# Performance work log

Measured on AMD Instinct MI355X. Metric: run time of the kernel, lower is better.

The kernel has to match this reference:

```python
import jax, jax.numpy as jnp
import numpy as np

N = 100000      # nodes
E = 1600000     # edges (avg degree 16)
D_IN = 128
CONV_SIZES = [64, 64]
FC_SIZES = [64, 32, 1]


def _glorot(key, shape):
    lim = np.sqrt(6.0 / (shape[0] + shape[1]))
    return jax.random.uniform(key, shape, jnp.float32, -lim, lim)


def setup_inputs() -> dict:
    key = jax.random.key(0)
    ks = jax.random.split(key, 2 + len(CONV_SIZES) + len(FC_SIZES))
    inp = {
        "x": jax.random.normal(ks[0], (N, D_IN), jnp.float32),
        "edge_index": jax.random.randint(ks[1], (2, E), 0, N, dtype=jnp.int64),
    }
    size = D_IN
    ki = 2
    for li, s in enumerate(CONV_SIZES):
        inp[f"cW{li}"] = _glorot(ks[ki], (size, s)); ki += 1
        inp[f"cb{li}"] = jnp.zeros((s,), jnp.float32)
        size = s
    for li, s in enumerate(FC_SIZES):
        inp[f"fW{li}"] = _glorot(ks[ki], (size, s)); ki += 1
        inp[f"fb{li}"] = jnp.zeros((s,), jnp.float32)
        size = s
    return inp


def gcn_conv(x, src, dst, W, b, n_nodes):
    """PyG GCNConv: symmetric normalization with added self-loops."""
    xl = x @ W  # [N, out]
    # degree including self-loop
    deg = jnp.zeros((n_nodes,), xl.dtype).at[dst].add(1.0) + 1.0
    dinv = jax.lax.rsqrt(deg)
    norm = dinv[src] * dinv[dst]                 # [E]
    msg = xl[src] * norm[:, None]                # gather + scale, [E, out]
    agg = jax.ops.segment_sum(msg, dst, num_segments=n_nodes)
    # self-loop contribution: norm = 1/deg
    return agg + xl * (1.0 / deg)[:, None] + b


def reference(x, edge_index, cW0, cb0, cW1, cb1, fW0, fb0, fW1, fb1, fW2, fb2):
    src, dst = edge_index[0], edge_index[1]
    h = jnp.tanh(gcn_conv(x, src, dst, cW0, cb0, N))
    h = jnp.tanh(gcn_conv(h, src, dst, cW1, cb1, N))
    h = jnp.tanh(h @ fW0 + fb0)
    h = jnp.tanh(h @ fW1 + fb1)
    return h @ fW2 + fb2  # [N, 1]
```

## Files before the change

kernel.cpp:

```cpp
#include <hip/hip_runtime.h>
#include <math.h>

#define N_NODES 100000
#define N_EDGES 1600000
#define NB     391
#define CHUNK  4096
#define NBLK_A 391

typedef unsigned short ushort_t;
typedef __attribute__((ext_vector_type(2))) float f2v;

__device__ inline unsigned short f2bf(float f) {
    unsigned u = __float_as_uint(f);
    unsigned r = (u + 0x7FFFu + ((u >> 16) & 1u)) >> 16;
    return (unsigned short)r;
}
__device__ inline void accp(f2v& a, unsigned u) {
    f2v t;
    t.x = __uint_as_float(u << 16);
    t.y = __uint_as_float(u & 0xFFFF0000u);
    a += t;
}
__device__ inline float fast_tanh(float x) {
    float e = __expf(2.0f * x);
    return fmaf(-2.0f, __builtin_amdgcn_rcpf(e + 1.0f), 1.0f);
}
__device__ inline void fma4(float4& acc, const float4 a,
                            const float4 w0, const float4 w1,
                            const float4 w2, const float4 w3) {
    acc.x = fmaf(a.x, w0.x, fmaf(a.y, w1.x, fmaf(a.z, w2.x, fmaf(a.w, w3.x, acc.x))));
    acc.y = fmaf(a.x, w0.y, fmaf(a.y, w1.y, fmaf(a.z, w2.y, fmaf(a.w, w3.y, acc.y))));
    acc.z = fmaf(a.x, w0.z, fmaf(a.y, w1.z, fmaf(a.z, w2.z, fmaf(a.w, w3.z, acc.z))));
    acc.w = fmaf(a.x, w0.w, fmaf(a.y, w1.w, fmaf(a.z, w2.w, fmaf(a.w, w3.w, acc.w))));
}


__global__ __launch_bounds__(256) void k_count(const int* __restrict__ dst,
                                               unsigned* __restrict__ cnt) {
    __shared__ unsigned h[NB];
    const int tid = threadIdx.x;
    const long e0 = (long)blockIdx.x * CHUNK;
    for (int i = tid; i < NB; i += 256) h[i] = 0u;
    __syncthreads();
    for (int i = tid; i < CHUNK; i += 256) {
        long e = e0 + i;
        if (e < N_EDGES) atomicAdd(&h[((unsigned)dst[e]) >> 8], 1u);
    }
    __syncthreads();
    for (int b = tid; b < NB; b += 256) cnt[b * NBLK_A + blockIdx.x] = h[b];
}

__global__ __launch_bounds__(512) void k_bucket_scan(unsigned* __restrict__ cnt,
                                                     unsigned* __restrict__ btot) {
    __shared__ unsigned s[512];
    const int tid = threadIdx.x;
    const int b = blockIdx.x;
    unsigned v = (tid < NBLK_A) ? cnt[b * NBLK_A + tid] : 0u;
    s[tid] = v;
    __syncthreads();
    for (int o = 1; o < 512; o <<= 1) {
        unsigned t = (tid >= o) ? s[tid - o] : 0u;
        __syncthreads();
        s[tid] += t;
        __syncthreads();
    }
    if (tid < NBLK_A) cnt[b * NBLK_A + tid] = s[tid] - v;
    if (tid == NBLK_A - 1) btot[b] = s[tid];
}

__global__ __launch_bounds__(512) void k_scan_bkt(const unsigned* __restrict__ btot,
                                                  unsigned* __restrict__ bktbase) {
    __shared__ unsigned s[512];
    const int tid = threadIdx.x;
    unsigned v = (tid < NB) ? btot[tid] : 0u;
    s[tid] = v;
    __syncthreads();
    for (int o = 1; o < 512; o <<= 1) {
        unsigned t = (tid >= o) ? s[tid - o] : 0u;
        __syncthreads();
        s[tid] += t;
        __syncthreads();
    }
    if (tid < NB) bktbase[tid] = s[tid] - v;
    if (tid == NB - 1) bktbase[NB] = s[tid];
}

__global__ __launch_bounds__(256) void k_bin(const int* __restrict__ src,
                                             const int* __restrict__ dst,
                                             const unsigned* __restrict__ cnt,
                                             const unsigned* __restrict__ bktbase,
                                             unsigned* __restrict__ binned) {
    __shared__ unsigned cntA[NB];
    __shared__ unsigned excl[NB];
    __shared__ unsigned gbase[NB];
    __shared__ unsigned scanbuf[512];
    __shared__ unsigned data[CHUNK];
    const int tid = threadIdx.x;
    const long e0 = (long)blockIdx.x * CHUNK;

    for (int i = tid; i < NB; i += 256) cntA[i] = 0u;
    __syncthreads();
    for (int i = tid; i < CHUNK; i += 256) {
        long e = e0 + i;
        if (e < N_EDGES) atomicAdd(&cntA[((unsigned)dst[e]) >> 8], 1u);
    }
    __syncthreads();
    scanbuf[tid] = (tid < NB) ? cntA[tid] : 0u;
    scanbuf[tid + 256] = (tid + 256 < NB) ? cntA[tid + 256] : 0u;
    __syncthreads();
    for (int o = 1; o < 512; o <<= 1) {
        unsigned v0 = (tid >= o) ? scanbuf[tid - o] : 0u;
        unsigned v1 = (tid + 256 >= o) ? scanbuf[tid + 256 - o] : 0u;
        __syncthreads();
        scanbuf[tid] += v0;
        scanbuf[tid + 256] += v1;
        __syncthreads();
    }
    for (int b = tid; b < NB; b += 256) {
        excl[b] = scanbuf[b] - cntA[b];
        gbase[b] = bktbase[b] + cnt[b * NBLK_A + blockIdx.x];
    }
    __syncthreads();
    for (int i = tid; i < NB; i += 256) cntA[i] = 0u;
    __syncthreads();
    for (int i = tid; i < CHUNK; i += 256) {
        long e = e0 + i;
        if (e < N_EDGES) {
            unsigned d = (unsigned)dst[e];
            unsigned b = d >> 8;
            unsigned slot = excl[b] + atomicAdd(&cntA[b], 1u);
            data[slot] = (((unsigned)src[e]) << 8) | (d & 255u);
        }
    }
    __syncthreads();
    const int w = tid >> 6, lane = tid & 63;
    for (int b = w; b < NB; b += 4) {
        unsigned c = cntA[b];
        unsigned sb = excl[b], gb = gbase[b];
        for (unsigned k = lane; k < c; k += 64)
            binned[gb + k] = data[sb + k];
    }
}

__global__ __launch_bounds__(256) void k_csr_fill2(const unsigned* __restrict__ binned,
                                                   const unsigned* __restrict__ bktbase,
                                                   unsigned* __restrict__ rowptr,
                                                   float* __restrict__ dinv,
                                                   int* __restrict__ ssrc) {
    __shared__ unsigned cnt[256];
    __shared__ unsigned s[256];
    __shared__ unsigned cur[256];
    const int b = blockIdx.x;
    const int tid = threadIdx.x;
    const int n0 = b * 256;
    const unsigned beg = bktbase[b], end = bktbase[b + 1];
    cnt[tid] = 0u;
    __syncthreads();
    for (unsigned i = beg + tid; i < end; i += 256)
        atomicAdd(&cnt[binned[i] & 255u], 1u);
    __syncthreads();
    const unsigned v = cnt[tid];
    s[tid] = v;
    __syncthreads();
    for (int o = 1; o < 256; o <<= 1) {
        unsigned t = (tid >= o) ? s[tid - o] : 0u;
        __syncthreads();
        s[tid] += t;
        __syncthreads();
    }
    const unsigned excl = s[tid] - v;
    const int node = n0 + tid;
    if (node < N_NODES) {
        rowptr[node] = beg + excl;
        dinv[node] = rsqrtf((float)(v + 1u));
        if (node == N_NODES - 1) rowptr[N_NODES] = end;
    }
    cur[tid] = beg + excl;
    __syncthreads();
    for (unsigned i = beg + tid; i < end; i += 256) {
        unsigned p = binned[i];
        unsigned pos = atomicAdd(&cur[p & 255u], 1u);
        ssrc[pos] = (int)(p >> 8);
    }
}


template<int K>
__global__ __launch_bounds__(256) void k_gemm_bf(const float* __restrict__ A,
                                                 const float* __restrict__ W,
                                                 const float* __restrict__ dinv,
                                                 ushort_t* __restrict__ C) {
    constexpr int OUT = 64;
    constexpr int BR = 64;
    constexpr int LDA = K + 4;
    __shared__ float Wld[K * OUT];
    __shared__ float Ald[BR * LDA];
    const int tid = threadIdx.x;
    const int row0 = blockIdx.x * BR;
    const int nrows = (N_NODES - row0 < BR) ? (N_NODES - row0) : BR;

    {
        const float4* W4 = reinterpret_cast<const float4*>(W);
        float4* Wl4 = reinterpret_cast<float4*>(Wld);
        for (int i = tid; i < K * OUT / 4; i += 256) Wl4[i] = W4[i];
        const float4* A4 = reinterpret_cast<const float4*>(A + (size_t)row0 * K);
        const int nv = nrows * (K / 4);
        for (int i = tid; i < nv; i += 256) {
            int r = i / (K / 4), q = i % (K / 4);
            *reinterpret_cast<float4*>(&Ald[r * LDA + q * 4]) = A4[i];
        }
    }
    __syncthreads();

    const int tr = tid >> 4;
    const int tc = tid & 15;
    const int r0 = tr * 4;
    float4 acc0 = {0,0,0,0}, acc1 = {0,0,0,0}, acc2 = {0,0,0,0}, acc3 = {0,0,0,0};
#pragma unroll 2
    for (int k4 = 0; k4 < K; k4 += 4) {
        const float4 a0 = *reinterpret_cast<const float4*>(&Ald[(r0 + 0) * LDA + k4]);
        const float4 a1 = *reinterpret_cast<const float4*>(&Ald[(r0 + 1) * LDA + k4]);
        const float4 a2 = *reinterpret_cast<const float4*>(&Ald[(r0 + 2) * LDA + k4]);
        const float4 a3 = *reinterpret_cast<const float4*>(&Ald[(r0 + 3) * LDA + k4]);
        const float4 w0 = *reinterpret_cast<const float4*>(&Wld[(k4 + 0) * OUT + tc * 4]);
        const float4 w1 = *reinterpret_cast<const float4*>(&Wld[(k4 + 1) * OUT + tc * 4]);
        const float4 w2 = *reinterpret_cast<const float4*>(&Wld[(k4 + 2) * OUT + tc * 4]);
        const float4 w3 = *reinterpret_cast<const float4*>(&Wld[(k4 + 3) * OUT + tc * 4]);
        fma4(acc0, a0, w0, w1, w2, w3);
        fma4(acc1, a1, w0, w1, w2, w3);
        fma4(acc2, a2, w0, w1, w2, w3);
        fma4(acc3, a3, w0, w1, w2, w3);
    }
    float4 accs[4] = {acc0, acc1, acc2, acc3};
#pragma unroll
    for (int i = 0; i < 4; ++i) {
        const int r = r0 + i;
        if (r < nrows) {
            const float di = dinv[row0 + r];
            ushort4 o;
            o.x = f2bf(accs[i].x * di);
            o.y = f2bf(accs[i].y * di);
            o.z = f2bf(accs[i].z * di);
            o.w = f2bf(accs[i].w * di);
            *reinterpret_cast<ushort4*>(&C[(size_t)(row0 + r) * OUT + tc * 4]) = o;
        }
    }
}

__global__ __launch_bounds__(256) void k_agg(const ushort_t* __restrict__ xlb,
                                             const float* __restrict__ dinv,
                                             const unsigned* __restrict__ rowptr,
                                             const int* __restrict__ ssrc,
                                             const float* __restrict__ bias,
                                             float* __restrict__ h) {
    const int node = blockIdx.x * 4 + (threadIdx.x >> 6);
    const int lane = threadIdx.x & 63;
    const int g = lane >> 4;
    const int l = lane & 15;
    const uint2* xb2 = reinterpret_cast<const uint2*>(xlb);

    const unsigned beg = rowptr[node], end = rowptr[node + 1];
    f2v a0 = {0.f, 0.f}, a1 = {0.f, 0.f};
    f2v b0 = {0.f, 0.f}, b1 = {0.f, 0.f};
    if (g == 0) {
        const uint2 v = xb2[(size_t)node * 16 + l];
        accp(a0, v.x); accp(a1, v.y);
    }
    unsigned j = beg + g;
    for (; j + 12 < end; j += 16) {
        const int s0i = ssrc[j];
        const int s1i = ssrc[j + 4];
        const int s2i = ssrc[j + 8];
        const int s3i = ssrc[j + 12];
        const uint2 v0 = xb2[(size_t)s0i * 16 + l];
        const uint2 v1 = xb2[(size_t)s1i * 16 + l];
        const uint2 v2 = xb2[(size_t)s2i * 16 + l];
        const uint2 v3 = xb2[(size_t)s3i * 16 + l];
        accp(a0, v0.x); accp(a1, v0.y);
        accp(b0, v1.x); accp(b1, v1.y);
        accp(a0, v2.x); accp(a1, v2.y);
        accp(b0, v3.x); accp(b1, v3.y);
    }
    for (; j < end; j += 4) {
        const uint2 v = xb2[(size_t)ssrc[j] * 16 + l];
        accp(a0, v.x); accp(a1, v.y);
    }
    a0 += b0; a1 += b1;
    float s0 = a0.x, s1 = a0.y, s2 = a1.x, s3 = a1.y;
    s0 += __shfl_xor(s0, 16); s1 += __shfl_xor(s1, 16);
    s2 += __shfl_xor(s2, 16); s3 += __shfl_xor(s3, 16);
    s0 += __shfl_xor(s0, 32); s1 += __shfl_xor(s1, 32);
    s2 += __shfl_xor(s2, 32); s3 += __shfl_xor(s3, 32);
    const float t01 = (g & 1) ? s1 : s0;
    const float t23 = (g & 1) ? s3 : s2;
    const float v = (g & 2) ? t23 : t01;
    const int f = l * 4 + g;
    const float r = fast_tanh(fmaf(v, dinv[node], bias[f]));
    h[(size_t)node * 64 + f] = r;
}

__global__ __launch_bounds__(256, 4) void k_fc(const float* __restrict__ h2,
                                               const float* __restrict__ fW0, const float* __restrict__ fb0,
                                               const float* __restrict__ fW1, const float* __restrict__ fb1,
                                               const float* __restrict__ fW2, const float* __restrict__ fb2,
                                               float* __restrict__ out) {
    constexpr int BR = 32;
    constexpr int LDH = 68;
    __shared__ float W0[64 * 64];
    __shared__ float W1[64 * 32];
    __shared__ float Hin[BR * LDH];
    __shared__ float Ht[BR * LDH];
    __shared__ float Hs[BR * 33];
    __shared__ float W2s[33];
    const int tid = threadIdx.x;
    {
        const float4* w04 = reinterpret_cast<const float4*>(fW0);
        float4* W04 = reinterpret_cast<float4*>(W0);
        for (int i = tid; i < 64 * 16; i += 256) W04[i] = w04[i];
        const float4* w14 = reinterpret_cast<const float4*>(fW1);
        float4* W14 = reinterpret_cast<float4*>(W1);
        for (int i = tid; i < 64 * 8; i += 256) W14[i] = w14[i];
        if (tid < 32) W2s[tid] = fW2[tid];
        if (tid == 32) W2s[32] = fb2[0];
    }
    const long row0 = (long)blockIdx.x * BR;
    {
        const float4* H4 = reinterpret_cast<const float4*>(h2 + row0 * 64);
        for (int i = tid; i < BR * 16; i += 256) {
            int r = i >> 4, q = i & 15;
            *reinterpret_cast<float4*>(&Hin[r * LDH + q * 4]) = H4[i];
        }
    }
    __syncthreads();

    {
        const int rp = tid >> 4;
        const int cq = tid & 15;
        const int r0 = rp * 2, r1 = r0 + 1;
        const float4 bias = reinterpret_cast<const float4*>(fb0)[cq];
        float4 acc0 = bias, acc1 = bias;
#pragma unroll 2
        for (int k4 = 0; k4 < 64; k4 += 4) {
            const float4 a0 = *reinterpret_cast<const float4*>(&Hin[r0 * LDH + k4]);
            const float4 a1 = *reinterpret_cast<const float4*>(&Hin[r1 * LDH + k4]);
            const float4 w0 = *reinterpret_cast<const float4*>(&W0[(k4 + 0) * 64 + cq * 4]);
            const float4 w1 = *reinterpret_cast<const float4*>(&W0[(k4 + 1) * 64 + cq * 4]);
            const float4 w2 = *reinterpret_cast<const float4*>(&W0[(k4 + 2) * 64 + cq * 4]);
            const float4 w3 = *reinterpret_cast<const float4*>(&W0[(k4 + 3) * 64 + cq * 4]);
            fma4(acc0, a0, w0, w1, w2, w3);
            fma4(acc1, a1, w0, w1, w2, w3);
        }
        float4 t0, t1;
        t0.x = fast_tanh(acc0.x); t0.y = fast_tanh(acc0.y);
        t0.z = fast_tanh(acc0.z); t0.w = fast_tanh(acc0.w);
        t1.x = fast_tanh(acc1.x); t1.y = fast_tanh(acc1.y);
        t1.z = fast_tanh(acc1.z); t1.w = fast_tanh(acc1.w);
        *reinterpret_cast<float4*>(&Ht[r0 * LDH + cq * 4]) = t0;
        *reinterpret_cast<float4*>(&Ht[r1 * LDH + cq * 4]) = t1;
    }
    __syncthreads();

    {
        const int r = tid >> 3;
        const int cq = tid & 7;
        const float4 bias = reinterpret_cast<const float4*>(fb1)[cq];
        float4 acc0 = bias;
#pragma unroll 2
        for (int k4 = 0; k4 < 64; k4 += 4) {
            const float4 a0 = *reinterpret_cast<const float4*>(&Ht[r * LDH + k4]);
            const float4 w0 = *reinterpret_cast<const float4*>(&W1[(k4 + 0) * 32 + cq * 4]);
            const float4 w1 = *reinterpret_cast<const float4*>(&W1[(k4 + 1) * 32 + cq * 4]);
            const float4 w2 = *reinterpret_cast<const float4*>(&W1[(k4 + 2) * 32 + cq * 4]);
            const float4 w3 = *reinterpret_cast<const float4*>(&W1[(k4 + 3) * 32 + cq * 4]);
            fma4(acc0, a0, w0, w1, w2, w3);
        }
        Hs[r * 33 + cq * 4 + 0] = fast_tanh(acc0.x);
        Hs[r * 33 + cq * 4 + 1] = fast_tanh(acc0.y);
        Hs[r * 33 + cq * 4 + 2] = fast_tanh(acc0.z);
        Hs[r * 33 + cq * 4 + 3] = fast_tanh(acc0.w);
    }
    __syncthreads();

    if (tid < BR) {
        float a = W2s[32];
        for (int k = 0; k < 32; ++k) a = fmaf(Hs[tid * 33 + k], W2s[k], a);
        out[row0 + tid] = a;
    }
}


extern "C" void kernel_launch(void* const* d_in, const int* in_sizes, int n_in,
                              void* d_out, int out_size, void* d_ws, size_t ws_size,
                              hipStream_t stream) {
    const float* x    = (const float*)d_in[0];
    const int*   eidx = (const int*)d_in[1];
    const float* cW0  = (const float*)d_in[2];
    const float* cb0  = (const float*)d_in[3];
    const float* cW1  = (const float*)d_in[4];
    const float* cb1  = (const float*)d_in[5];
    const float* fW0  = (const float*)d_in[6];
    const float* fb0  = (const float*)d_in[7];
    const float* fW1  = (const float*)d_in[8];
    const float* fb1  = (const float*)d_in[9];
    const float* fW2  = (const float*)d_in[10];
    const float* fb2  = (const float*)d_in[11];
    float* out = (float*)d_out;

    const int* src = eidx;
    const int* dst = eidx + N_EDGES;

    char* ws = (char*)d_ws;
    unsigned* rowptr  = (unsigned*)(ws);
    float*    dinv    = (float*)   (ws + 400016);
    unsigned* cnt     = (unsigned*)(ws + 800016);
    unsigned* btot    = (unsigned*)(ws + 1411552);
    unsigned* bktbase = (unsigned*)(ws + 1413120);
    int*      ssrc    = (int*)     (ws + 1414688);
    ushort_t* xlb     = (ushort_t*)(ws + 7814688);
    unsigned* binned  = (unsigned*)(ws + 20614688);
    float*    bufB    = (float*)   (ws + 27014688);

    const int gRow = N_NODES / 32;
    const int gGemm = (N_NODES + 63) / 64;
    const int gAgg = N_NODES / 4;

    k_count<<<NBLK_A, 256, 0, stream>>>(dst, cnt);
    k_bucket_scan<<<NB, 512, 0, stream>>>(cnt, btot);
    k_scan_bkt<<<1, 512, 0, stream>>>(btot, bktbase);
    k_bin<<<NBLK_A, 256, 0, stream>>>(src, dst, cnt, bktbase, binned);
    k_csr_fill2<<<NB, 256, 0, stream>>>(binned, bktbase, rowptr, dinv, ssrc);

    k_gemm_bf<128><<<gGemm, 256, 0, stream>>>(x, cW0, dinv, xlb);
    k_agg<<<gAgg, 256, 0, stream>>>(xlb, dinv, rowptr, ssrc, cb0, bufB);
    k_gemm_bf<64><<<gGemm, 256, 0, stream>>>(bufB, cW1, dinv, xlb);
    k_agg<<<gAgg, 256, 0, stream>>>(xlb, dinv, rowptr, ssrc, cb1, bufB);
    k_fc<<<gRow, 256, 0, stream>>>(bufB, fW0, fb0, fW1, fb1, fW2, fb2, out);
}
```

Baseline: 256.2 us.

## Store hidden activations in bf16 and widen aggregation gathers to 16 bytes

The aggregation kernel now writes its tanh output as bf16 instead of fp32. The second GCN GEMM and the FC kernel get new bf16-input loaders that unpack to fp32 in shared memory. The aggregation is restructured so each lane gathers 16-byte uint4 chunks (8 features) with 8 edge groups per node, followed by a three-stage shuffle reduction. This halves activation write and read traffic and uses wider gather loads, at the cost of extra bf16 rounding of intermediate activations and fewer independent loads in flight per lane.

```diff
diff --git a/kernel.cpp b/kernel.cpp
--- a/kernel.cpp
+++ b/kernel.cpp
@@ -8,18 +8,15 @@
 #define NBLK_A 391
 
 typedef unsigned short ushort_t;
-typedef __attribute__((ext_vector_type(2))) float f2v;
 
 __device__ inline unsigned short f2bf(float f) {
     unsigned u = __float_as_uint(f);
     unsigned r = (u + 0x7FFFu + ((u >> 16) & 1u)) >> 16;
     return (unsigned short)r;
 }
-__device__ inline void accp(f2v& a, unsigned u) {
-    f2v t;
-    t.x = __uint_as_float(u << 16);
-    t.y = __uint_as_float(u & 0xFFFF0000u);
-    a += t;
+__device__ inline void acc2(float& a0, float& a1, unsigned u) {
+    a0 += __uint_as_float(u << 16);
+    a1 += __uint_as_float(u & 0xFFFF0000u);
 }
 __device__ inline float fast_tanh(float x) {
     float e = __expf(2.0f * x);
@@ -32,6 +29,12 @@
     acc.y = fmaf(a.x, w0.y, fmaf(a.y, w1.y, fmaf(a.z, w2.y, fmaf(a.w, w3.y, acc.y))));
     acc.z = fmaf(a.x, w0.z, fmaf(a.y, w1.z, fmaf(a.z, w2.z, fmaf(a.w, w3.z, acc.z))));
     acc.w = fmaf(a.x, w0.w, fmaf(a.y, w1.w, fmaf(a.z, w2.w, fmaf(a.w, w3.w, acc.w))));
+}
+__device__ inline void bf8_to_f32(float* p, uint4 v) {
+    p[0] = __uint_as_float(v.x << 16); p[1] = __uint_as_float(v.x & 0xFFFF0000u);
+    p[2] = __uint_as_float(v.y << 16); p[3] = __uint_as_float(v.y & 0xFFFF0000u);
+    p[4] = __uint_as_float(v.z << 16); p[5] = __uint_as_float(v.z & 0xFFFF0000u);
+    p[6] = __uint_as_float(v.w << 16); p[7] = __uint_as_float(v.w & 0xFFFF0000u);
 }
 
 
@@ -215,7 +218,7 @@
     const int tr = tid >> 4;
     const int tc = tid & 15;
     const int r0 = tr * 4;
-    float4 acc0 = {0,0,0,0}, acc1 = {0,0,0,0}, acc2 = {0,0,0,0}, acc3 = {0,0,0,0};
+    float4 acc0 = {0,0,0,0}, acc1 = {0,0,0,0}, acc2v = {0,0,0,0}, acc3 = {0,0,0,0};
 #pragma unroll 2
     for (int k4 = 0; k4 < K; k4 += 4) {
         const float4 a0 = *reinterpret_cast<const float4*>(&Ald[(r0 + 0) * LDA + k4]);
@@ -228,10 +231,10 @@
         const float4 w3 = *reinterpret_cast<const float4*>(&Wld[(k4 + 3) * OUT + tc * 4]);
         fma4(acc0, a0, w0, w1, w2, w3);
         fma4(acc1, a1, w0, w1, w2, w3);
-        fma4(acc2, a2, w0, w1, w2, w3);
+        fma4(acc2v, a2, w0, w1, w2, w3);
         fma4(acc3, a3, w0, w1, w2, w3);
     }
-    float4 accs[4] = {acc0, acc1, acc2, acc3};
+    float4 accs[4] = {acc0, acc1, acc2v, acc3};
 #pragma unroll
     for (int i = 0; i < 4; ++i) {
         const int r = r0 + i;
@@ -242,7 +245,69 @@
             o.y = f2bf(accs[i].y * di);
             o.z = f2bf(accs[i].z * di);
             o.w = f2bf(accs[i].w * di);
-            *reinterpret_cast<ushort4*>(&C[(size_t)(row0 + r) * OUT + tc * 4]) = o;
+            *reinterpret_cast<ushort4*>(&C[(size_t)(row0 + r) * 64 + tc * 4]) = o;
+        }
+    }
+}
+
+__global__ __launch_bounds__(256) void k_gemm_bfin(const ushort_t* __restrict__ A,
+                                                   const float* __restrict__ W,
+                                                   const float* __restrict__ dinv,
+                                                   ushort_t* __restrict__ C) {
+    constexpr int K = 64;
+    constexpr int OUT = 64;
+    constexpr int BR = 64;
+    constexpr int LDA = K + 4;
+    __shared__ float Wld[K * OUT];
+    __shared__ float Ald[BR * LDA];
+    const int tid = threadIdx.x;
+    const int row0 = blockIdx.x * BR;
+    const int nrows = (N_NODES - row0 < BR) ? (N_NODES - row0) : BR;
+
+    {
+        const float4* W4 = reinterpret_cast<const float4*>(W);
+        float4* Wl4 = reinterpret_cast<float4*>(Wld);
+        for (int i = tid; i < K * OUT / 4; i += 256) Wl4[i] = W4[i];
+        const uint4* A4 = reinterpret_cast<const uint4*>(A + (size_t)row0 * K);
+        const int nv = nrows * 8;
+        for (int i = tid; i < nv; i += 256) {
+            int r = i >> 3, q = i & 7;
+            bf8_to_f32(&Ald[r * LDA + q * 8], A4[i]);
+        }
+    }
+    __syncthreads();
+
+    const int tr = tid >> 4;
+    const int tc = tid & 15;
+    const int r0 = tr * 4;
+    float4 acc0 = {0,0,0,0}, acc1 = {0,0,0,0}, acc2v = {0,0,0,0}, acc3 = {0,0,0,0};
+#pragma unroll 2
+    for (int k4 = 0; k4 < K; k4 += 4) {
+        const float4 a0 = *reinterpret_cast<const float4*>(&Ald[(r0 + 0) * LDA + k4]);
+        const float4 a1 = *reinterpret_cast<const float4*>(&Ald[(r0 + 1) * LDA + k4]);
+        const float4 a2 = *reinterpret_cast<const float4*>(&Ald[(r0 + 2) * LDA + k4]);
+        const float4 a3 = *reinterpret_cast<const float4*>(&Ald[(r0 + 3) * LDA + k4]);
+        const float4 w0 = *reinterpret_cast<const float4*>(&Wld[(k4 + 0) * OUT + tc * 4]);
+        const float4 w1 = *reinterpret_cast<const float4*>(&Wld[(k4 + 1) * OUT + tc * 4]);
+        const float4 w2 = *reinterpret_cast<const float4*>(&Wld[(k4 + 2) * OUT + tc * 4]);
+        const float4 w3 = *reinterpret_cast<const float4*>(&Wld[(k4 + 3) * OUT + tc * 4]);
+        fma4(acc0, a0, w0, w1, w2, w3);
+        fma4(acc1, a1, w0, w1, w2, w3);
+        fma4(acc2v, a2, w0, w1, w2, w3);
+        fma4(acc3, a3, w0, w1, w2, w3);
+    }
+    float4 accs[4] = {acc0, acc1, acc2v, acc3};
+#pragma unroll
+    for (int i = 0; i < 4; ++i) {
+        const int r = r0 + i;
+        if (r < nrows) {
+            const float di = dinv[row0 + r];
+            ushort4 o;
+            o.x = f2bf(accs[i].x * di);
+            o.y = f2bf(accs[i].y * di);
+            o.z = f2bf(accs[i].z * di);
+            o.w = f2bf(accs[i].w * di);
+            *reinterpret_cast<ushort4*>(&C[(size_t)(row0 + r) * 64 + tc * 4]) = o;
         }
     }
 }
@@ -252,54 +317,67 @@
                                              const unsigned* __restrict__ rowptr,
                                              const int* __restrict__ ssrc,
                                              const float* __restrict__ bias,
-                                             float* __restrict__ h) {
+                                             ushort_t* __restrict__ hb) {
     const int node = blockIdx.x * 4 + (threadIdx.x >> 6);
     const int lane = threadIdx.x & 63;
-    const int g = lane >> 4;
-    const int l = lane & 15;
-    const uint2* xb2 = reinterpret_cast<const uint2*>(xlb);
+    const int g = lane >> 3;
+    const int l = lane & 7;
+    const uint4* xb4 = reinterpret_cast<const uint4*>(xlb);
 
     const unsigned beg = rowptr[node], end = rowptr[node + 1];
-    f2v a0 = {0.f, 0.f}, a1 = {0.f, 0.f};
-    f2v b0 = {0.f, 0.f}, b1 = {0.f, 0.f};
+    float a[8] = {0.f,0.f,0.f,0.f,0.f,0.f,0.f,0.f};
+    float b[8] = {0.f,0.f,0.f,0.f,0.f,0.f,0.f,0.f};
     if (g == 0) {
-        const uint2 v = xb2[(size_t)node * 16 + l];
-        accp(a0, v.x); accp(a1, v.y);
+        const uint4 v = xb4[(size_t)node * 8 + l];
+        acc2(a[0], a[1], v.x); acc2(a[2], a[3], v.y);
+        acc2(a[4], a[5], v.z); acc2(a[6], a[7], v.w);
     }
     unsigned j = beg + g;
-    for (; j + 12 < end; j += 16) {
-        const int s0i = ssrc[j];
-        const int s1i = ssrc[j + 4];
-        const int s2i = ssrc[j + 8];
-        const int s3i = ssrc[j + 12];
-        const uint2 v0 = xb2[(size_t)s0i * 16 + l];
-        const uint2 v1 = xb2[(size_t)s1i * 16 + l];
-        const uint2 v2 = xb2[(size_t)s2i * 16 + l];
-        const uint2 v3 = xb2[(size_t)s3i * 16 + l];
-        accp(a0, v0.x); accp(a1, v0.y);
-        accp(b0, v1.x); accp(b1, v1.y);
-        accp(a0, v2.x); accp(a1, v2.y);
-        accp(b0, v3.x); accp(b1, v3.y);
-    }
-    for (; j < end; j += 4) {
-        const uint2 v = xb2[(size_t)ssrc[j] * 16 + l];
-        accp(a0, v.x); accp(a1, v.y);
-    }
-    a0 += b0; a1 += b1;
-    float s0 = a0.x, s1 = a0.y, s2 = a1.x, s3 = a1.y;
-    s0 += __shfl_xor(s0, 16); s1 += __shfl_xor(s1, 16);
-    s2 += __shfl_xor(s2, 16); s3 += __shfl_xor(s3, 16);
-    s0 += __shfl_xor(s0, 32); s1 += __shfl_xor(s1, 32);
-    s2 += __shfl_xor(s2, 32); s3 += __shfl_xor(s3, 32);
-    const float t01 = (g & 1) ? s1 : s0;
-    const float t23 = (g & 1) ? s3 : s2;
-    const float v = (g & 2) ? t23 : t01;
-    const int f = l * 4 + g;
-    const float r = fast_tanh(fmaf(v, dinv[node], bias[f]));
-    h[(size_t)node * 64 + f] = r;
-}
-
-__global__ __launch_bounds__(256, 4) void k_fc(const float* __restrict__ h2,
+    for (; j + 8 < end; j += 16) {
+        const int s0 = ssrc[j];
+        const int s1 = ssrc[j + 8];
+        const uint4 v0 = xb4[(size_t)s0 * 8 + l];
+        const uint4 v1 = xb4[(size_t)s1 * 8 + l];
+        acc2(a[0], a[1], v0.x); acc2(a[2], a[3], v0.y);
+        acc2(a[4], a[5], v0.z); acc2(a[6], a[7], v0.w);
+        acc2(b[0], b[1], v1.x); acc2(b[2], b[3], v1.y);
+        acc2(b[4], b[5], v1.z); acc2(b[6], b[7], v1.w);
+    }
+    if (j < end) {
+        const uint4 v = xb4[(size_t)ssrc[j] * 8 + l];
+        acc2(a[0], a[1], v.x); acc2(a[2], a[3], v.y);
+        acc2(a[4], a[5], v.z); acc2(a[6], a[7], v.w);
+    }
+#pragma unroll
+    for (int i = 0; i < 8; ++i) a[i] += b[i];
+#pragma unroll
+    for (int i = 0; i < 8; ++i) {
+        a[i] += __shfl_xor(a[i], 8);
+        a[i] += __shfl_xor(a[i], 16);
+        a[i] += __shfl_xor(a[i], 32);
+    }
+    if (g == 0) {
+        const float di = dinv[node];
+        const float4 b0 = reinterpret_cast<const float4*>(bias)[l * 2];
+        const float4 b1 = reinterpret_cast<const float4*>(bias)[l * 2 + 1];
+        float r0 = fast_tanh(fmaf(a[0], di, b0.x));
+        float r1 = fast_tanh(fmaf(a[1], di, b0.y));
+        float r2 = fast_tanh(fmaf(a[2], di, b0.z));
+        float r3 = fast_tanh(fmaf(a[3], di, b0.w));
+        float r4 = fast_tanh(fmaf(a[4], di, b1.x));
+        float r5 = fast_tanh(fmaf(a[5], di, b1.y));
+        float r6 = fast_tanh(fmaf(a[6], di, b1.z));
+        float r7 = fast_tanh(fmaf(a[7], di, b1.w));
+        uint4 o;
+        o.x = (unsigned)f2bf(r0) | ((unsigned)f2bf(r1) << 16);
+        o.y = (unsigned)f2bf(r2) | ((unsigned)f2bf(r3) << 16);
+        o.z = (unsigned)f2bf(r4) | ((unsigned)f2bf(r5) << 16);
+        o.w = (unsigned)f2bf(r6) | ((unsigned)f2bf(r7) << 16);
+        reinterpret_cast<uint4*>(hb)[(size_t)node * 8 + l] = o;
+    }
+}
+
+__global__ __launch_bounds__(256, 4) void k_fc(const ushort_t* __restrict__ h2,
                                                const float* __restrict__ fW0, const float* __restrict__ fb0,
                                                const float* __restrict__ fW1, const float* __restrict__ fb1,
                                                const float* __restrict__ fW2, const float* __restrict__ fb2,
@@ -325,10 +403,10 @@
     }
     const long row0 = (long)blockIdx.x * BR;
     {
-        const float4* H4 = reinterpret_cast<const float4*>(h2 + row0 * 64);
-        for (int i = tid; i < BR * 16; i += 256) {
-            int r = i >> 4, q = i & 15;
-            *reinterpret_cast<float4*>(&Hin[r * LDH + q * 4]) = H4[i];
+        const uint4* H4 = reinterpret_cast<const uint4*>(h2 + row0 * 64);
+        if (tid < BR * 8) {
+            int r = tid >> 3, q = tid & 7;
+            bf8_to_f32(&Hin[r * LDH + q * 8], H4[tid]);
         }
     }
     __syncthreads();
@@ -418,7 +496,7 @@
     int*      ssrc    = (int*)     (ws + 1414688);
     ushort_t* xlb     = (ushort_t*)(ws + 7814688);
     unsigned* binned  = (unsigned*)(ws + 20614688);
-    float*    bufB    = (float*)   (ws + 27014688);
+    ushort_t* hb      = (ushort_t*)(ws + 27014688);
 
     const int gRow = N_NODES / 32;
     const int gGemm = (N_NODES + 63) / 64;
@@ -431,8 +509,8 @@
     k_csr_fill2<<<NB, 256, 0, stream>>>(binned, bktbase, rowptr, dinv, ssrc);
 
     k_gemm_bf<128><<<gGemm, 256, 0, stream>>>(x, cW0, dinv, xlb);
-    k_agg<<<gAgg, 256, 0, stream>>>(xlb, dinv, rowptr, ssrc, cb0, bufB);
-    k_gemm_bf<64><<<gGemm, 256, 0, stream>>>(bufB, cW1, dinv, xlb);
-    k_agg<<<gAgg, 256, 0, stream>>>(xlb, dinv, rowptr, ssrc, cb1, bufB);
-    k_fc<<<gRow, 256, 0, stream>>>(bufB, fW0, fb0, fW1, fb1, fW2, fb2, out);
-}
+    k_agg<<<gAgg, 256, 0, stream>>>(xlb, dinv, rowptr, ssrc, cb0, hb);
+    k_gemm_bfin<<<gGemm, 256, 0, stream>>>(hb, cW1, dinv, xlb);
+    k_agg<<<gAgg, 256, 0, stream>>>(xlb, dinv, rowptr, ssrc, cb1, hb);
+    k_fc<<<gRow, 256, 0, stream>>>(hb, fW0, fb0, fW1, fb1, fW2, fb2, out);
+}
```

New measurement: 249.8 us. 2.5% less time.
